# Kernel optimization log

Measured on AMD Instinct MI355X. Metric: run time of the kernel, lower is better.

Reference implementation:

```python
import jax, jax.numpy as jnp
import numpy as np

BLOCK = 32          # MX spec: 32-element blocks share one E8M0 scale
E4M3_MAX = 448.0    # max finite value of float8_e4m3fn
EMAX_E4M3 = 8       # exponent of largest e4m3 binade (448 = 1.75 * 2^8)
MIN_NORM_EXP = -6   # smallest normal exponent of e4m3 (subnormals below)
MANT_BITS = 3


def _round_e4m3(v):
    """Emulate round-to-nearest cast to float8_e4m3fn (saturating)."""
    a = jnp.abs(v)
    # exponent of each element, clamped so subnormals use the -6 binade step
    e = jnp.clip(jnp.floor(jnp.log2(jnp.maximum(a, 1e-30))), MIN_NORM_EXP, EMAX_E4M3)
    step = jnp.exp2(e - MANT_BITS)          # quantization step in this binade
    q = jnp.round(a / step) * step
    q = jnp.minimum(q, E4M3_MAX)            # saturate (e4m3fn has no inf)
    return jnp.sign(v) * q


def quantize_mx_dequant(x):
    """MX quantize a 2D [M, K] tensor with E8M0 per-32-block scales to e4m3,
    then dequantize (q * scale). Math-equivalent to the xq/x_scales pair fed
    into torch._scaled_mm."""
    M, K = x.shape
    xb = x.reshape(M, K // BLOCK, BLOCK)
    amax = jnp.max(jnp.abs(xb), axis=-1, keepdims=True)
    # E8M0 shared scale: 2^(floor(log2(amax)) - emax_elem), clamped to E8M0 range
    exp = jnp.floor(jnp.log2(jnp.maximum(amax, 1e-30))) - EMAX_E4M3
    exp = jnp.clip(exp, -127.0, 127.0)
    scale = jnp.exp2(exp)
    q = _round_e4m3(xb / scale)
    return (q * scale).reshape(M, K)


def setup_inputs() -> dict:
    key = jax.random.key(0)
    k1, k2, k3 = jax.random.split(key, 3)
    x = jax.random.normal(k1, (8192, 4096), dtype=jnp.float32)
    weight = jax.random.normal(k2, (4096, 4096), dtype=jnp.float32) * 0.02
    bias = jax.random.normal(k3, (4096,), dtype=jnp.float32) * 0.02
    return {"x": x, "weight": weight, "bias": bias}


def reference(x, weight, bias):
    x_2d = x.reshape(-1, x.shape[-1])            # [M, K]
    xd = quantize_mx_dequant(x_2d)               # MX-quantized activations
    wd = quantize_mx_dequant(weight)             # MX-quantized weights (buffer wq/w_scales)
    out = xd @ wd.T + bias                       # scaled matmul + bias
    return out.reshape(*x.shape[:-1], out.shape[-1])
```

## Files before the change

kernel.cpp:

```cpp
#include <hip/hip_runtime.h>

typedef __attribute__((ext_vector_type(8))) short bf16x8;
typedef __attribute__((ext_vector_type(4))) float f32x4;
typedef __attribute__((ext_vector_type(4))) unsigned short u16x4;

#define BM 256
#define BN 256
#define BK 64

__device__ __forceinline__ float pow2i(int e) {
  if (e >= -126) return __uint_as_float((unsigned)(e + 127) << 23);
  return __uint_as_float(0x00400000u >> (-126 - e));
}

__device__ __forceinline__ float qdq_e4m3(float x, float inv, float scale) {
  float s = x * inv;
  float a = fabsf(s);
  int ee = (int)((__float_as_uint(a) >> 23) & 0xffu) - 127;
  ee = ee < -6 ? -6 : (ee > 8 ? 8 : ee);
  float istep = __uint_as_float((unsigned)(130 - ee) << 23);
  float step  = __uint_as_float((unsigned)(124 + ee) << 23);
  float q = rintf(a * istep) * step;
  q = fminf(q, 448.0f);
  return copysignf(q, s) * scale;
}

__device__ __forceinline__ u16x4 qdq_pack(float4 v) {
  float am = fmaxf(fmaxf(fabsf(v.x), fabsf(v.y)), fmaxf(fabsf(v.z), fabsf(v.w)));
  am = fmaxf(am, __shfl_xor(am, 1));
  am = fmaxf(am, __shfl_xor(am, 2));
  am = fmaxf(am, __shfl_xor(am, 4));
  int e = (int)((__float_as_uint(am) >> 23) & 0xffu) - 135;
  e = e < -127 ? -127 : (e > 127 ? 127 : e);
  float scale = pow2i(e);
  float inv   = pow2i(-e);
  u16x4 o;
  o[0] = (unsigned short)(__float_as_uint(qdq_e4m3(v.x, inv, scale)) >> 16);
  o[1] = (unsigned short)(__float_as_uint(qdq_e4m3(v.y, inv, scale)) >> 16);
  o[2] = (unsigned short)(__float_as_uint(qdq_e4m3(v.z, inv, scale)) >> 16);
  o[3] = (unsigned short)(__float_as_uint(qdq_e4m3(v.w, inv, scale)) >> 16);
  return o;
}

__global__ void quant_mx(const float4* __restrict__ in, u16x4* __restrict__ outq,
                         long long n4) {
  const long long base = (long long)blockIdx.x * blockDim.x + threadIdx.x;
  const long long stride = (long long)gridDim.x * blockDim.x;
  const long long i0 = base, i1 = base + stride, i2 = base + 2 * stride, i3 = base + 3 * stride;
  float4 v0, v1, v2, v3;
  if (i0 < n4) v0 = in[i0];
  if (i1 < n4) v1 = in[i1];
  if (i2 < n4) v2 = in[i2];
  if (i3 < n4) v3 = in[i3];
  u16x4 o0, o1, o2, o3;
  if (i0 < n4) o0 = qdq_pack(v0);
  if (i1 < n4) o1 = qdq_pack(v1);
  if (i2 < n4) o2 = qdq_pack(v2);
  if (i3 < n4) o3 = qdq_pack(v3);
  if (i0 < n4) outq[i0] = o0;
  if (i1 < n4) outq[i1] = o1;
  if (i2 < n4) outq[i2] = o2;
  if (i3 < n4) outq[i3] = o3;
}

__device__ __forceinline__ void gload_lds16(const void* g, void* l) {
  __builtin_amdgcn_global_load_lds(
      (const __attribute__((address_space(1))) unsigned int*)g,
      (__attribute__((address_space(3))) unsigned int*)l, 16, 0, 0);
}

#define BAR() do { asm volatile("" ::: "memory"); \
                   __builtin_amdgcn_s_barrier();  \
                   asm volatile("" ::: "memory"); } while (0)
#define WAIT_VM0() asm volatile("s_waitcnt vmcnt(0)" ::: "memory")
#define WAIT_VM2() asm volatile("s_waitcnt vmcnt(2)" ::: "memory")
#define WAIT_VM4() asm volatile("s_waitcnt vmcnt(4)" ::: "memory")

__global__ __launch_bounds__(512, 2) void gemm_mx(
    const unsigned short* __restrict__ A, const unsigned short* __restrict__ B,
    const float* __restrict__ bias, float* __restrict__ C,
    int M, int N, int K) {
  __shared__ __align__(16) unsigned short As[2][BM * BK];
  __shared__ __align__(16) unsigned short Bs[2][BN * BK];

  const int tid = threadIdx.x;
  const int l  = tid & 63, w = tid >> 6;
  const int wr = w >> 2, wc = w & 3;
  const int rr = l & 15, kq = l >> 4;

  const int nbx = N / BN;
  const int bid = blockIdx.x;
  const int cpx = gridDim.x >> 3;
  const int swz = (bid & 7) * cpx + (bid >> 3);
  const int by = swz / nbx, bx = swz % nbx;

  const unsigned short* gA = A + (size_t)by * BM * K;
  const unsigned short* gB = B + (size_t)bx * BN * K;

  f32x4 acc[8][4] = {};

  const int swx   = (rr & 7) * 8;
  const int kofs0 = (kq * 8) ^ swx;
  const int kofs1 = (32 + kq * 8) ^ swx;

#define STAGE(G, L, CH, KT) do {                                   \
    int _ch = (CH);                                                \
    int _row = _ch >> 3;                                           \
    int _c16 = (_ch & 7) ^ (_row & 7);                             \
    gload_lds16((G) + (size_t)_row * K + (KT) + _c16 * 8,          \
                (L) + _ch * 8);                                    \
  } while (0)

  bf16x8 af[4][2], bg[4][2];

#define READ_A(MH) _Pragma("unroll")                               \
  for (int m = 0; m < 4; ++m) {                                    \
    const int rb = (wr * 128 + ((MH) * 4 + m) * 16 + rr) * BK;     \
    af[m][0] = *(const bf16x8*)&Ac[rb + kofs0];                    \
    af[m][1] = *(const bf16x8*)&Ac[rb + kofs1];                    \
  }
#define READ_B(NH) _Pragma("unroll")                               \
  for (int n = 0; n < 2; ++n) {                                    \
    const int rb = (wc * 64 + ((NH) * 2 + n) * 16 + rr) * BK;      \
    bg[(NH) * 2 + n][0] = *(const bf16x8*)&Bc[rb + kofs0];         \
    bg[(NH) * 2 + n][1] = *(const bf16x8*)&Bc[rb + kofs1];         \
  }
#define MFMA16(MH, NH)                                             \
  __builtin_amdgcn_s_setprio(1);                                   \
  _Pragma("unroll")                                                \
  for (int kk = 0; kk < 2; ++kk)                                   \
    _Pragma("unroll")                                              \
    for (int m = 0; m < 4; ++m)                                    \
      _Pragma("unroll")                                            \
      for (int n = 0; n < 2; ++n)                                  \
        acc[(MH)*4+m][(NH)*2+n] = __builtin_amdgcn_mfma_f32_16x16x32_bf16( \
            af[m][kk], bg[(NH)*2+n][kk], acc[(MH)*4+m][(NH)*2+n], 0, 0, 0);\
  __builtin_amdgcn_s_setprio(0);

  {
    unsigned short* Ad = As[0];
    unsigned short* Bd = Bs[0];
    STAGE(gB, Bd, tid,        0); STAGE(gB, Bd, tid + 512,  0);
    STAGE(gB, Bd, tid + 1024, 0); STAGE(gB, Bd, tid + 1536, 0);
    STAGE(gA, Ad, tid,        0); STAGE(gA, Ad, tid + 1024, 0);
    STAGE(gA, Ad, tid + 512,  0); STAGE(gA, Ad, tid + 1536, 0);
    WAIT_VM0();
    BAR();
  }

  const int NTK = K / BK;
  int cur = 0;
  for (int t = 0; t < NTK; ++t) {
    const bool pf = (t + 1 < NTK);
    const int ktn = (t + 1) * BK;
    unsigned short* Ac = As[cur];
    unsigned short* Bc = Bs[cur];
    unsigned short* An = As[cur ^ 1];
    unsigned short* Bn = Bs[cur ^ 1];

    READ_A(0) READ_B(0)
    if (pf) { STAGE(gB, Bn, tid, ktn); STAGE(gB, Bn, tid + 512, ktn); }
    BAR();
    MFMA16(0, 0)
    BAR();

    READ_B(1)
    if (pf) { STAGE(gB, Bn, tid + 1024, ktn); STAGE(gB, Bn, tid + 1536, ktn); }
    BAR();
    MFMA16(0, 1)
    if (pf) WAIT_VM4(); else WAIT_VM0();
    BAR();

    READ_A(1)
    if (pf) { STAGE(gA, An, tid, ktn); STAGE(gA, An, tid + 1024, ktn); }
    BAR();
    MFMA16(1, 1)
    BAR();

    if (pf) { STAGE(gA, An, tid + 512, ktn); STAGE(gA, An, tid + 1536, ktn); }
    MFMA16(1, 0)
    if (pf) WAIT_VM2(); else WAIT_VM0();
    BAR();

    cur ^= 1;
  }

#pragma unroll
  for (int ni = 0; ni < 4; ++ni) {
    const int col = bx * BN + wc * 64 + ni * 16 + rr;
    const float bv = bias[col];
#pragma unroll
    for (int mi = 0; mi < 8; ++mi) {
      const int row0 = by * BM + wr * 128 + mi * 16 + kq * 4;
#pragma unroll
      for (int j = 0; j < 4; ++j) {
        C[(size_t)(row0 + j) * N + col] = acc[mi][ni][j] + bv;
      }
    }
  }
}

extern "C" void kernel_launch(void* const* d_in, const int* in_sizes, int n_in,
                              void* d_out, int out_size, void* d_ws, size_t ws_size,
                              hipStream_t stream) {
  const float* x    = (const float*)d_in[0];
  const float* wt   = (const float*)d_in[1];
  const float* bias = (const float*)d_in[2];
  float* out = (float*)d_out;

  const int N = in_sizes[2];
  const int K = (int)((long long)in_sizes[1] / N);
  const int M = (int)((long long)in_sizes[0] / K);

  unsigned short* xq = (unsigned short*)d_ws;
  unsigned short* wq = xq + (size_t)M * K;

  long long nx4 = (long long)M * K / 4;
  long long nw4 = (long long)N * K / 4;
  int gx = (int)((nx4 + 4LL * 256 - 1) / (4LL * 256));
  int gw = (int)((nw4 + 4LL * 256 - 1) / (4LL * 256));
  quant_mx<<<gx, 256, 0, stream>>>((const float4*)x,  (u16x4*)xq, nx4);
  quant_mx<<<gw, 256, 0, stream>>>((const float4*)wt, (u16x4*)wq, nw4);

  dim3 grid((M / BM) * (N / BN));
  gemm_mx<<<grid, 512, 0, stream>>>(xq, wq, bias, out, M, N, K);
}
```

Measured before the change: 534.3 us.

## Restructure GEMM main loop into 8-phase ping-pong with register-prefetched fragments

The GEMM main loop now handles two K-tiles per iteration. It prologue-loads both LDS buffers and keeps A/B fragments in multiple register sets, so LDS reads for the next quarter overlap the MFMA work on the current one, with finer-grained vmcnt waits. The two quantization launches are merged into one kernel with one float4 per thread, which removes a launch but drops the four-way load batching. The change raises register pressure and assumes NTK is even.

```diff
diff --git a/kernel.cpp b/kernel.cpp
--- a/kernel.cpp
+++ b/kernel.cpp
@@ -42,25 +42,14 @@
   return o;
 }
 
-__global__ void quant_mx(const float4* __restrict__ in, u16x4* __restrict__ outq,
-                         long long n4) {
-  const long long base = (long long)blockIdx.x * blockDim.x + threadIdx.x;
-  const long long stride = (long long)gridDim.x * blockDim.x;
-  const long long i0 = base, i1 = base + stride, i2 = base + 2 * stride, i3 = base + 3 * stride;
-  float4 v0, v1, v2, v3;
-  if (i0 < n4) v0 = in[i0];
-  if (i1 < n4) v1 = in[i1];
-  if (i2 < n4) v2 = in[i2];
-  if (i3 < n4) v3 = in[i3];
-  u16x4 o0, o1, o2, o3;
-  if (i0 < n4) o0 = qdq_pack(v0);
-  if (i1 < n4) o1 = qdq_pack(v1);
-  if (i2 < n4) o2 = qdq_pack(v2);
-  if (i3 < n4) o3 = qdq_pack(v3);
-  if (i0 < n4) outq[i0] = o0;
-  if (i1 < n4) outq[i1] = o1;
-  if (i2 < n4) outq[i2] = o2;
-  if (i3 < n4) outq[i3] = o3;
+__global__ void quant_mx2(const float4* __restrict__ x,  u16x4* __restrict__ xq, long long nx4,
+                          const float4* __restrict__ wt, u16x4* __restrict__ wq, long long nw4) {
+  long long i = (long long)blockIdx.x * blockDim.x + threadIdx.x;
+  long long total = nx4 + nw4;
+  if (i >= total) return;
+  const float4* in = (i < nx4) ? (x + i) : (wt + (i - nx4));
+  u16x4* out = (i < nx4) ? (xq + i) : (wq + (i - nx4));
+  *out = qdq_pack(*in);
 }
 
 __device__ __forceinline__ void gload_lds16(const void* g, void* l) {
@@ -73,8 +62,8 @@
                    __builtin_amdgcn_s_barrier();  \
                    asm volatile("" ::: "memory"); } while (0)
 #define WAIT_VM0() asm volatile("s_waitcnt vmcnt(0)" ::: "memory")
-#define WAIT_VM2() asm volatile("s_waitcnt vmcnt(2)" ::: "memory")
 #define WAIT_VM4() asm volatile("s_waitcnt vmcnt(4)" ::: "memory")
+#define WAIT_VM6() asm volatile("s_waitcnt vmcnt(6)" ::: "memory")
 
 __global__ __launch_bounds__(512, 2) void gemm_mx(
     const unsigned short* __restrict__ A, const unsigned short* __restrict__ B,
@@ -96,6 +85,9 @@
 
   const unsigned short* gA = A + (size_t)by * BM * K;
   const unsigned short* gB = B + (size_t)bx * BN * K;
+
+  unsigned short* As0 = As[0]; unsigned short* As1 = As[1];
+  unsigned short* Bs0 = Bs[0]; unsigned short* Bs1 = Bs[1];
 
   f32x4 acc[8][4] = {};
 
@@ -111,21 +103,18 @@
                 (L) + _ch * 8);                                    \
   } while (0)
 
-  bf16x8 af[4][2], bg[4][2];
-
-#define READ_A(MH) _Pragma("unroll")                               \
-  for (int m = 0; m < 4; ++m) {                                    \
-    const int rb = (wr * 128 + ((MH) * 4 + m) * 16 + rr) * BK;     \
-    af[m][0] = *(const bf16x8*)&Ac[rb + kofs0];                    \
-    af[m][1] = *(const bf16x8*)&Ac[rb + kofs1];                    \
-  }
-#define READ_B(NH) _Pragma("unroll")                               \
-  for (int n = 0; n < 2; ++n) {                                    \
-    const int rb = (wc * 64 + ((NH) * 2 + n) * 16 + rr) * BK;      \
-    bg[(NH) * 2 + n][0] = *(const bf16x8*)&Bc[rb + kofs0];         \
-    bg[(NH) * 2 + n][1] = *(const bf16x8*)&Bc[rb + kofs1];         \
-  }
-#define MFMA16(MH, NH)                                             \
+  bf16x8 af0[4][2], af1[4][2], bgA[2][2], bgB[2][2], bgN[2][2];
+
+#define RD_A8(ARR, MI, HALF, LP) do {                              \
+    const int rb = (wr * 128 + (HALF) * 64 + (MI) * 16 + rr) * BK; \
+    ARR[MI][0] = *(const bf16x8*)&LP[rb + kofs0];                  \
+    ARR[MI][1] = *(const bf16x8*)&LP[rb + kofs1]; } while (0)
+#define RD_B8(ARR, NI, HALF, LP) do {                              \
+    const int rb = (wc * 64 + (HALF) * 32 + (NI) * 16 + rr) * BK;  \
+    ARR[NI][0] = *(const bf16x8*)&LP[rb + kofs0];                  \
+    ARR[NI][1] = *(const bf16x8*)&LP[rb + kofs1]; } while (0)
+
+#define MFMAQ(MB, NB, AF, BG)                                      \
   __builtin_amdgcn_s_setprio(1);                                   \
   _Pragma("unroll")                                                \
   for (int kk = 0; kk < 2; ++kk)                                   \
@@ -133,56 +122,81 @@
     for (int m = 0; m < 4; ++m)                                    \
       _Pragma("unroll")                                            \
       for (int n = 0; n < 2; ++n)                                  \
-        acc[(MH)*4+m][(NH)*2+n] = __builtin_amdgcn_mfma_f32_16x16x32_bf16( \
-            af[m][kk], bg[(NH)*2+n][kk], acc[(MH)*4+m][(NH)*2+n], 0, 0, 0);\
+        acc[(MB)*4+m][(NB)+n] = __builtin_amdgcn_mfma_f32_16x16x32_bf16( \
+            AF[m][kk], BG[n][kk], acc[(MB)*4+m][(NB)+n], 0, 0, 0); \
   __builtin_amdgcn_s_setprio(0);
 
-  {
-    unsigned short* Ad = As[0];
-    unsigned short* Bd = Bs[0];
-    STAGE(gB, Bd, tid,        0); STAGE(gB, Bd, tid + 512,  0);
-    STAGE(gB, Bd, tid + 1024, 0); STAGE(gB, Bd, tid + 1536, 0);
-    STAGE(gA, Ad, tid,        0); STAGE(gA, Ad, tid + 1024, 0);
-    STAGE(gA, Ad, tid + 512,  0); STAGE(gA, Ad, tid + 1536, 0);
-    WAIT_VM0();
-    BAR();
-  }
+  STAGE(gA, As0, tid, 0);        STAGE(gA, As0, tid + 512, 0);
+  STAGE(gA, As0, tid + 1024, 0); STAGE(gA, As0, tid + 1536, 0);
+  STAGE(gB, Bs0, tid, 0);        STAGE(gB, Bs0, tid + 512, 0);
+  STAGE(gB, Bs0, tid + 1024, 0); STAGE(gB, Bs0, tid + 1536, 0);
+  STAGE(gA, As1, tid, BK);        STAGE(gA, As1, tid + 512, BK);
+  STAGE(gA, As1, tid + 1024, BK); STAGE(gA, As1, tid + 1536, BK);
+  STAGE(gB, Bs1, tid, BK);        STAGE(gB, Bs1, tid + 512, BK);
+  STAGE(gB, Bs1, tid + 1024, BK); STAGE(gB, Bs1, tid + 1536, BK);
+  WAIT_VM0();
+  BAR();
+  RD_A8(af0, 0, 0, As0); RD_A8(af0, 1, 0, As0);
+  RD_A8(af0, 2, 0, As0); RD_A8(af0, 3, 0, As0);
+  RD_B8(bgA, 0, 0, Bs0); RD_B8(bgA, 1, 0, Bs0);
 
   const int NTK = K / BK;
-  int cur = 0;
-  for (int t = 0; t < NTK; ++t) {
-    const bool pf = (t + 1 < NTK);
-    const int ktn = (t + 1) * BK;
-    unsigned short* Ac = As[cur];
-    unsigned short* Bc = Bs[cur];
-    unsigned short* An = As[cur ^ 1];
-    unsigned short* Bn = Bs[cur ^ 1];
-
-    READ_A(0) READ_B(0)
-    if (pf) { STAGE(gB, Bn, tid, ktn); STAGE(gB, Bn, tid + 512, ktn); }
-    BAR();
-    MFMA16(0, 0)
-    BAR();
-
-    READ_B(1)
-    if (pf) { STAGE(gB, Bn, tid + 1024, ktn); STAGE(gB, Bn, tid + 1536, ktn); }
-    BAR();
-    MFMA16(0, 1)
-    if (pf) WAIT_VM4(); else WAIT_VM0();
-    BAR();
-
-    READ_A(1)
-    if (pf) { STAGE(gA, An, tid, ktn); STAGE(gA, An, tid + 1024, ktn); }
-    BAR();
-    MFMA16(1, 1)
-    BAR();
-
-    if (pf) { STAGE(gA, An, tid + 512, ktn); STAGE(gA, An, tid + 1536, ktn); }
-    MFMA16(1, 0)
-    if (pf) WAIT_VM2(); else WAIT_VM0();
-    BAR();
-
-    cur ^= 1;
+  const int NIT = NTK / 2;
+  for (int it = 0; it < NIT; ++it) {
+    const bool last = (it == NIT - 1);
+    const int kt2 = (2 * it + 2) * BK, kt3 = (2 * it + 3) * BK;
+
+    RD_B8(bgB, 0, 1, Bs0); RD_B8(bgB, 1, 1, Bs0); RD_A8(af1, 0, 1, As0);
+    BAR();
+    MFMAQ(0, 0, af0, bgA)
+    BAR();
+
+    RD_A8(af1, 1, 1, As0); RD_A8(af1, 2, 1, As0); RD_A8(af1, 3, 1, As0);
+    if (!last) { STAGE(gB, Bs0, tid + 1024, kt2); STAGE(gB, Bs0, tid + 1536, kt2); }
+    BAR();
+    MFMAQ(0, 2, af0, bgB)
+    if (last) { WAIT_VM0(); } else { WAIT_VM4(); }
+    BAR();
+
+    RD_A8(af0, 0, 0, As1); RD_A8(af0, 1, 0, As1); RD_A8(af0, 2, 0, As1);
+    if (!last) { STAGE(gA, As0, tid, kt2);        STAGE(gA, As0, tid + 512, kt2);
+                 STAGE(gA, As0, tid + 1024, kt2); STAGE(gA, As0, tid + 1536, kt2); }
+    BAR();
+    MFMAQ(1, 2, af1, bgB)
+    if (last) { WAIT_VM0(); } else { WAIT_VM6(); }
+    BAR();
+
+    RD_A8(af0, 3, 0, As1); RD_B8(bgN, 0, 0, Bs1); RD_B8(bgN, 1, 0, Bs1);
+    if (!last) { STAGE(gB, Bs0, tid, kt2); STAGE(gB, Bs0, tid + 512, kt2); }
+    BAR();
+    MFMAQ(1, 0, af1, bgA)
+    BAR();
+
+    RD_B8(bgB, 0, 1, Bs1); RD_B8(bgB, 1, 1, Bs1); RD_A8(af1, 0, 1, As1);
+    BAR();
+    MFMAQ(0, 0, af0, bgN)
+    BAR();
+
+    RD_A8(af1, 1, 1, As1); RD_A8(af1, 2, 1, As1); RD_A8(af1, 3, 1, As1);
+    if (!last) { STAGE(gB, Bs1, tid + 1024, kt3); STAGE(gB, Bs1, tid + 1536, kt3); }
+    BAR();
+    MFMAQ(0, 2, af0, bgB)
+    if (last) { WAIT_VM0(); } else { WAIT_VM4(); }
+    BAR();
+
+    RD_A8(af0, 0, 0, As0); RD_A8(af0, 1, 0, As0); RD_A8(af0, 2, 0, As0);
+    if (!last) { STAGE(gA, As1, tid, kt3);        STAGE(gA, As1, tid + 512, kt3);
+                 STAGE(gA, As1, tid + 1024, kt3); STAGE(gA, As1, tid + 1536, kt3); }
+    BAR();
+    MFMAQ(1, 2, af1, bgB)
+    if (last) { WAIT_VM0(); } else { WAIT_VM6(); }
+    BAR();
+
+    RD_A8(af0, 3, 0, As0); RD_B8(bgA, 0, 0, Bs0); RD_B8(bgA, 1, 0, Bs0);
+    if (!last) { STAGE(gB, Bs1, tid, kt3); STAGE(gB, Bs1, tid + 512, kt3); }
+    BAR();
+    MFMAQ(1, 0, af1, bgN)
+    BAR();
   }
 
 #pragma unroll
@@ -217,10 +231,10 @@
 
   long long nx4 = (long long)M * K / 4;
   long long nw4 = (long long)N * K / 4;
-  int gx = (int)((nx4 + 4LL * 256 - 1) / (4LL * 256));
-  int gw = (int)((nw4 + 4LL * 256 - 1) / (4LL * 256));
-  quant_mx<<<gx, 256, 0, stream>>>((const float4*)x,  (u16x4*)xq, nx4);
-  quant_mx<<<gw, 256, 0, stream>>>((const float4*)wt, (u16x4*)wq, nw4);
+  long long tot = nx4 + nw4;
+  int gq = (int)((tot + 255) / 256);
+  quant_mx2<<<gq, 256, 0, stream>>>((const float4*)x, (u16x4*)xq, nx4,
+                                    (const float4*)wt, (u16x4*)wq, nw4);
 
   dim3 grid((M / BM) * (N / BN));
   gemm_mx<<<grid, 512, 0, stream>>>(xq, wq, bias, out, M, N, K);
```

After: 663.8 us. 24.2% more time.
